# Optimization experiments

Hardware: AMD Instinct MI355X
Metric: run time of the kernel (lower is better)

The kernel has to match this reference:

```python
import jax, jax.numpy as jnp
import numpy as np

NUM_CLASSES = 80
SCORE_THR = 0.2
NMS_THR = 0.3
MAX_PER_IMAGE = 100
TOPK_PER_CLASS = 100  # cap on pre-NMS candidates per (image, class); >= max_per_image
ANCHOR_MASK = [[6, 7, 8], [3, 4, 5], [0, 1, 2]]
COCO_ANCHORS = np.array([[10, 13], [16, 30], [33, 23], [30, 61], [62, 45],
                         [59, 119], [116, 90], [156, 198], [373, 326]], dtype=np.float32)


def yolo_head(feats, layer_anchors, num_classes, input_shape):
    # feats: [B, 3*(5+C), gh, gw]
    B = feats.shape[0]
    gh, gw = feats.shape[2], feats.shape[3]
    na = layer_anchors.shape[0]
    f = feats.reshape(B, na, num_classes + 5, gh, gw).transpose(0, 3, 4, 1, 2)  # [B,gh,gw,3,5+C]
    gy, gx = jnp.meshgrid(jnp.arange(gh), jnp.arange(gw), indexing='ij')
    grid = jnp.stack([gx, gy], axis=-1).astype(f.dtype)[None, :, :, None, :]  # [1,gh,gw,1,2]
    # literal translation: divide by tensor([gh, gw]) (square grids in practice)
    box_xy = (jax.nn.sigmoid(f[..., :2]) + grid) / jnp.array([gh, gw], f.dtype)
    box_wh = jnp.exp(f[..., 2:4]) * layer_anchors[None, None, None, :, :] / input_shape[None, None, None, None, :]
    conf = jax.nn.sigmoid(f[..., 4:5])
    probs = jax.nn.sigmoid(f[..., 5:])
    return box_xy, box_wh, conf, probs


def yolo_correct_boxes(box_xy, box_wh, input_shape, image_shape):
    box_yx = box_xy[..., ::-1]
    box_hw = box_wh[..., ::-1]
    new_shape = jnp.round(image_shape * jnp.min(input_shape / image_shape))
    offset = (input_shape - new_shape) / 2.0 / input_shape
    scale = input_shape / new_shape
    box_yx = (box_yx - offset) * scale
    box_hw = box_hw * scale
    mins = box_yx - box_hw / 2.0
    maxes = box_yx + box_hw / 2.0
    boxes = jnp.concatenate([mins, maxes], axis=-1)  # (ymin, xmin, ymax, xmax)
    return boxes * jnp.concatenate([image_shape, image_shape])


def decode_layer(feats, layer_anchors, input_shape, image_shape):
    box_xy, box_wh, conf, probs = yolo_head(feats, layer_anchors, NUM_CLASSES, input_shape)
    boxes = yolo_correct_boxes(box_xy, box_wh, input_shape, image_shape)  # [B,gh,gw,3,4]
    B = feats.shape[0]
    return boxes.reshape(B, -1, 4), (conf * probs).reshape(B, -1, NUM_CLASSES)


def pairwise_iou(b):
    # b: [K,4] (y1,x1,y2,x2)
    y1, x1, y2, x2 = b[:, 0], b[:, 1], b[:, 2], b[:, 3]
    area = jnp.maximum(y2 - y1, 0) * jnp.maximum(x2 - x1, 0)
    iy1 = jnp.maximum(y1[:, None], y1[None, :])
    ix1 = jnp.maximum(x1[:, None], x1[None, :])
    iy2 = jnp.minimum(y2[:, None], y2[None, :])
    ix2 = jnp.minimum(x2[:, None], x2[None, :])
    inter = jnp.maximum(iy2 - iy1, 0) * jnp.maximum(ix2 - ix1, 0)
    return inter / (area[:, None] + area[None, :] - inter + 1e-9)


def greedy_nms(boxes, valid):
    # boxes [K,4] sorted by descending score; valid [K] bool. Returns keep mask [K].
    K = boxes.shape[0]
    iou = jax.lax.stop_gradient(pairwise_iou(boxes))
    idx = jnp.arange(K)
    def body(i, sup):
        keep_i = valid[i] & (~sup[i])
        return sup | (keep_i & (iou[i] > NMS_THR) & (idx > i))
    sup = jax.lax.fori_loop(0, K, body, jnp.zeros((K,), bool))
    return valid & (~sup)


def setup_inputs() -> dict:
    key = jax.random.key(0)
    k0, k1, k2 = jax.random.split(key, 3)
    B, F = 16, 3 * (5 + NUM_CLASSES)
    feat0 = jax.random.normal(k0, (B, F, 19, 19), jnp.float32)
    feat1 = jax.random.normal(k1, (B, F, 38, 38), jnp.float32)
    feat2 = jax.random.normal(k2, (B, F, 76, 76), jnp.float32)
    anchors = jnp.asarray(COCO_ANCHORS)
    image_shape = jnp.array([480.0, 640.0], jnp.float32)
    return {"feat0": feat0, "feat1": feat1, "feat2": feat2,
            "anchors": anchors, "image_shape": image_shape}


def reference(feat0, feat1, feat2, anchors, image_shape):
    input_shape = jnp.array([feat0.shape[2] * 32, feat0.shape[3] * 32], jnp.float32)
    feats = [feat0, feat1, feat2]
    boxes_l, scores_l = [], []
    for l in range(3):
        b, s = decode_layer(feats[l], anchors[np.array(ANCHOR_MASK[l])], input_shape, image_shape)
        boxes_l.append(b)
        scores_l.append(s)
    boxes = jnp.concatenate(boxes_l, axis=1)    # [B,N,4]
    scores = jnp.concatenate(scores_l, axis=1)  # [B,N,C]
    B = scores.shape[0]
    sc = scores.transpose(0, 2, 1)              # [B,C,N]
    top_s, top_i = jax.lax.top_k(sc, TOPK_PER_CLASS)              # [B,C,K]
    top_b = jnp.take_along_axis(boxes[:, None, :, :], top_i[..., None], axis=2)  # [B,C,K,4]
    valid = top_s >= SCORE_THR
    keep = jax.vmap(jax.vmap(greedy_nms))(top_b, valid)           # [B,C,K]
    cand = jnp.where(keep, top_s, -1.0)
    flat_s = cand.reshape(B, -1)                 # [B, C*K]
    flat_b = top_b.reshape(B, -1, 4)
    sel_s, sel_i = jax.lax.top_k(flat_s, MAX_PER_IMAGE)           # [B,100]
    sel_b = jnp.take_along_axis(flat_b, sel_i[..., None], axis=1)  # [B,100,4]
    sel_c = (sel_i // TOPK_PER_CLASS).astype(jnp.float32)
    # dets: (ymin, xmin, ymax, xmax, score, class); score == -1 marks padding
    return jnp.concatenate([sel_b, sel_s[..., None], sel_c[..., None]], axis=-1)
```

## Files before the change

### kernel.cpp

```cpp
#include <hip/hip_runtime.h>
#include <hip/hip_bf16.h>


#define NTOT   22743
#define NCLS   80
#define TOPK   100
#define KPAD   22752
#define NVEC   2842
#define Q_L1   17328
#define Q_L0   21660
#define SCORE_THR 0.2f
#define NMS_THR   0.3f

__device__ __forceinline__ float sig_exact(float x) {
    return 1.0f / (1.0f + expf(-x));
}
__device__ __forceinline__ float sig_fast(float x) {
    return __builtin_amdgcn_rcpf(1.0f + __expf(-x));
}

__global__ __launch_bounds__(256) void k_decode(
    const float* __restrict__ f0, const float* __restrict__ f1,
    const float* __restrict__ f2, const float* __restrict__ anchors,
    const float* __restrict__ imshape, float4* __restrict__ boxes,
    float* __restrict__ conf_q, int total) {
    int gid = blockIdx.x * 256 + threadIdx.x;
    if (gid >= total) return;
    int b = gid / NTOT; int p = gid - b * NTOT;

    const float* f; int ghw, gw, l, off, a, s;
    if (p < 1083)      { f=f0; off=0;    ghw=361;  gw=19; l=0; int r=p;      a=r/361;  s=r-a*361;  }
    else if (p < 5415) { f=f1; off=1083; ghw=1444; gw=38; l=1; int r=p-1083; a=r/1444; s=r-a*1444; }
    else               { f=f2; off=5415; ghw=5776; gw=76; l=2; int r=p-5415; a=r/5776; s=r-a*5776; }
    int y = s / gw, x = s - y * gw;

    const float* q = f + ((size_t)(b * 255 + a * 85) * ghw + s);
    float tx = q[0], ty = q[ghw], tw = q[2*ghw], th = q[3*ghw], tc = q[4*ghw];

    int arow = (2 - l) * 3 + a;
    float aw = anchors[arow * 2], ah = anchors[arow * 2 + 1];
    float imh = imshape[0], imw = imshape[1];
    float gf = (float)gw;

    float bxx = (sig_exact(tx) + (float)x) / gf;
    float bxy = (sig_exact(ty) + (float)y) / gf;
    float bw  = expf(tw) * aw / 608.0f;
    float bh  = expf(th) * ah / 608.0f;

    float r  = fminf(608.0f / imh, 608.0f / imw);
    float nh = rintf(imh * r), nw = rintf(imw * r);
    float offy = (608.0f - nh) / 2.0f / 608.0f;
    float offx = (608.0f - nw) / 2.0f / 608.0f;
    float scy = 608.0f / nh, scx = 608.0f / nw;

    float cy = (bxy - offy) * scy;
    float cx = (bxx - offx) * scx;
    float hh = bh * scy, ww = bw * scx;

    int n = off + 3 * s + a;
    boxes[(size_t)b * NTOT + n] =
        make_float4((cy - hh / 2.0f) * imh, (cx - ww / 2.0f) * imw,
                    (cy + hh / 2.0f) * imh, (cx + ww / 2.0f) * imw);
    int qi = (l == 2) ? (a * 5776 + s)
           : (l == 1) ? (Q_L1 + a * 1444 + s)
                      : (Q_L0 + a * 361 + s);
    conf_q[(size_t)b * KPAD + qi] = sig_exact(tc);
}

#define SEG_A  346560
#define SEG_AB 433200
#define SEG_T  519840
__global__ __launch_bounds__(256) void k_score(
    const float* __restrict__ f0, const float* __restrict__ f1,
    const float* __restrict__ f2, const float* __restrict__ conf_q,
    unsigned short* __restrict__ keybuf, int total) {
    int gid = blockIdx.x * 256 + threadIdx.x;
    if (gid >= total) return;
    const int b = gid / SEG_T;
    const int w = gid - b * SEG_T;

    if (w < SEG_AB) {
        const float* f; int a, c, s, qbase, ghw;
        if (w < SEG_A) {
            a = w / 115520; int r = w - a * 115520;
            c = r / 1444;   s = (r - c * 1444) * 4;
            f = f2; ghw = 5776; qbase = a * 5776;
        } else {
            int t = w - SEG_A;
            a = t / 28880;  int r = t - a * 28880;
            c = r / 361;    s = (r - c * 361) * 4;
            f = f1; ghw = 1444; qbase = Q_L1 + a * 1444;
        }
        const float4 lg = *(const float4*)(f + ((size_t)(b * 255 + a * 85 + 5 + c) * ghw + s));
        const float4 cf = *(const float4*)(conf_q + (size_t)b * KPAD + qbase + s);
        ushort4 k;
        k.x = (unsigned short)(__float_as_uint(cf.x * sig_fast(lg.x)) >> 16);
        k.y = (unsigned short)(__float_as_uint(cf.y * sig_fast(lg.y)) >> 16);
        k.z = (unsigned short)(__float_as_uint(cf.z * sig_fast(lg.z)) >> 16);
        k.w = (unsigned short)(__float_as_uint(cf.w * sig_fast(lg.w)) >> 16);
        *(ushort4*)(keybuf + ((size_t)(b * NCLS + c)) * KPAD + qbase + s) = k;
    } else {
        int t = w - SEG_AB;
        int a = t / 28880;  int r = t - a * 28880;
        int c = r / 361;    int s = r - c * 361;
        int qi = Q_L0 + a * 361 + s;
        float lg = f0[((size_t)(b * 255 + a * 85 + 5 + c) * 361 + s)];
        float cf = conf_q[(size_t)b * KPAD + qi];
        keybuf[((size_t)(b * NCLS + c)) * KPAD + qi] =
            (unsigned short)(__float_as_uint(cf * sig_fast(lg)) >> 16);
    }
}

__device__ void find_pivot(unsigned* hist, int H, unsigned target,
                           unsigned* suf, unsigned* sh_p, unsigned* sh_above) {
    const int tid = threadIdx.x;
    const int per = H >> 8;
    if (tid < 256) {
        unsigned acc = 0;
        for (int u = 0; u < per; ++u) acc += hist[tid * per + u];
        suf[tid] = acc;
    }
    __syncthreads();
    for (int off = 1; off < 256; off <<= 1) {
        unsigned v = 0;
        if (tid < 256) v = (tid + off < 256) ? suf[tid + off] : 0u;
        __syncthreads();
        if (tid < 256) suf[tid] += v;
        __syncthreads();
    }
    if (tid < 256) {
        unsigned mysuf = suf[tid];
        unsigned nxt = (tid == 255) ? 0u : suf[tid + 1];
        if (mysuf >= target && nxt < target) {
            unsigned above = nxt;
            for (int h = tid * per + per - 1; h >= tid * per; --h) {
                unsigned c2 = above + hist[h];
                if (c2 >= target) { *sh_p = (unsigned)h; *sh_above = above; break; }
                above = c2;
            }
        }
    }
    __syncthreads();
}

template <int TPB>
__device__ void sortT512(unsigned long long* buf) {
    const int tid = threadIdx.x;
    for (int k = 2; k <= 512; k <<= 1)
        for (int j = k >> 1; j > 0; j >>= 1) {
            __syncthreads();
            for (int i = tid; i < 512; i += TPB) {
                int ixj = i ^ j;
                if (ixj > i) {
                    unsigned long long a = buf[i], bb = buf[ixj];
                    bool desc = ((i & k) == 0);
                    if (desc ? (a < bb) : (a > bb)) { buf[i] = bb; buf[ixj] = a; }
                }
            }
        }
    __syncthreads();
}

__device__ __forceinline__ void collect_cand(
    int b, int c, int q, const float* __restrict__ f0,
    const float* __restrict__ f1, const float* __restrict__ f2,
    const float* __restrict__ conf_q, unsigned long long* buf,
    unsigned* sh_cnt) {
    int a, s, nbase, ghw;
    const float* f;
    if (q < Q_L1)      { a = q / 5776;  s = q - a * 5776;  f = f2; ghw = 5776; nbase = 5415; }
    else if (q < Q_L0) { int r = q - Q_L1; a = r / 1444; s = r - a * 1444; f = f1; ghw = 1444; nbase = 1083; }
    else               { int r = q - Q_L0; a = r / 361;  s = r - a * 361;  f = f0; ghw = 361;  nbase = 0;    }
    float t  = f[((size_t)(b * 255 + a * 85 + 5 + c)) * ghw + s];
    float cf = conf_q[(size_t)b * KPAD + q];
    float sce = cf * sig_exact(t);
    int n = nbase + 3 * s + a;
    unsigned slot = atomicAdd(sh_cnt, 1u);
    if (slot < 512)
        buf[slot] = (((unsigned long long)__float_as_uint(sce)) << 32)
                    | (unsigned)(~n);
}

__global__ __launch_bounds__(512, 8) void k_topk(
    const float* __restrict__ f0, const float* __restrict__ f1,
    const float* __restrict__ f2, const float* __restrict__ conf_q,
    const unsigned short* __restrict__ keybuf,
    const float4* __restrict__ boxes, float* __restrict__ top_s,
    float4* __restrict__ top_b) {
    __shared__ unsigned int histp[4096];
    __shared__ unsigned long long buf[512];
    __shared__ unsigned int wsum[4];
    __shared__ unsigned int sh_p, sh_above, sh_cnt;

    const int tid = threadIdx.x;
    const int row = blockIdx.x;
    const int b = row / NCLS, c = row - b * NCLS;
    const unsigned short* kr = keybuf + (size_t)row * KPAD;
    const uint4* kv = (const uint4*)kr;

    for (int i = tid; i < 4096; i += 512) histp[i] = 0;
    if (tid == 0) sh_cnt = 0;
    __syncthreads();

    for (int g = tid; g < NVEC; g += 512) {
        uint4 v = kv[g];
        unsigned ks[8] = { v.x & 0xFFFFu, v.x >> 16, v.y & 0xFFFFu, v.y >> 16,
                           v.z & 0xFFFFu, v.z >> 16, v.w & 0xFFFFu, v.w >> 16 };
        #pragma unroll
        for (int j = 0; j < 8; ++j)
            atomicAdd(&histp[ks[j] >> 2], 1u << (((ks[j] >> 1) & 1u) * 16));
    }
    if (tid < NTOT - NVEC * 8) {
        unsigned k = kr[NVEC * 8 + tid];
        atomicAdd(&histp[k >> 2], 1u << (((k >> 1) & 1u) * 16));
    }
    __syncthreads();

    {
        const int lane = tid & 63;
        unsigned own = 0;
        if (tid < 256) {
            #pragma unroll
            for (int u = 0; u < 16; ++u) {
                unsigned w = histp[tid * 16 + u];
                own += (w & 0xFFFFu) + (w >> 16);
            }
        }
        unsigned acc = own;
        #pragma unroll
        for (int d = 1; d < 64; d <<= 1) {
            unsigned v = __shfl_down(acc, d, 64);
            if (lane + d < 64) acc += v;
        }
        if (tid < 256 && lane == 0) wsum[tid >> 6] = acc;
        __syncthreads();
        if (tid < 256) {
            unsigned tail = 0;
            for (int w2 = (tid >> 6) + 1; w2 < 4; ++w2) tail += wsum[w2];
            unsigned suft = acc + tail;
            unsigned nxt  = suft - own;
            if (suft >= TOPK && nxt < TOPK) {
                unsigned above = nxt;
                for (int bb = 31; bb >= 0; --bb) {
                    unsigned w = histp[tid * 16 + (bb >> 1)];
                    unsigned cnt = (bb & 1) ? (w >> 16) : (w & 0xFFFFu);
                    if (above + cnt >= TOPK) {
                        sh_p = (unsigned)(tid * 32 + bb); sh_above = above; break;
                    }
                    above += cnt;
                }
            }
        }
        __syncthreads();
    }
    const unsigned kthr = sh_p > 0 ? ((sh_p - 1) << 1) : 0u;

    for (int g = tid; g < NVEC; g += 512) {
        uint4 v = kv[g];
        unsigned ks[8] = { v.x & 0xFFFFu, v.x >> 16, v.y & 0xFFFFu, v.y >> 16,
                           v.z & 0xFFFFu, v.z >> 16, v.w & 0xFFFFu, v.w >> 16 };
        #pragma unroll
        for (int j = 0; j < 8; ++j)
            if (ks[j] >= kthr)
                collect_cand(b, c, g * 8 + j, f0, f1, f2, conf_q, buf, &sh_cnt);
    }
    if (tid < NTOT - NVEC * 8) {
        int q = NVEC * 8 + tid;
        if ((unsigned)kr[q] >= kthr)
            collect_cand(b, c, q, f0, f1, f2, conf_q, buf, &sh_cnt);
    }
    __syncthreads();
    unsigned M = sh_cnt; if (M > 512) M = 512;
    for (int i = tid; i < 512; i += 512) if ((unsigned)i >= M) buf[i] = 0ull;
    __syncthreads();
    sortT512<512>(buf);

    if (tid < TOPK) {
        unsigned long long k = buf[tid];
        unsigned bits = (unsigned)(k >> 32);
        int n = (int)(~(unsigned)k);
        top_s[row * TOPK + tid] = __uint_as_float(bits);
        top_b[row * TOPK + tid] = boxes[(size_t)b * NTOT + n];
    }
}

__global__ __launch_bounds__(256) void k_nms(
    const float* __restrict__ top_s, const float4* __restrict__ top_b,
    float* __restrict__ cand) {
    const int lane = threadIdx.x & 63;
    const int row  = blockIdx.x * 4 + (threadIdx.x >> 6);
    const float4* bb = top_b + (size_t)row * TOPK;
    const float*  ss = top_s + (size_t)row * TOPK;

    const int j0 = lane, j1 = lane + 64;
    const bool v1 = (j1 < TOPK);
    float4 B0 = bb[j0];
    float  s0 = ss[j0];
    float4 B1 = v1 ? bb[j1] : make_float4(0.f, 0.f, 0.f, 0.f);
    float  s1 = v1 ? ss[j1] : -1.0f;
    float ar0 = fmaxf(B0.z - B0.x, 0.f) * fmaxf(B0.w - B0.y, 0.f);
    float ar1 = fmaxf(B1.z - B1.x, 0.f) * fmaxf(B1.w - B1.y, 0.f);
    int sup0 = 0, sup1 = 0;

    for (int i = 0; i < TOPK; ++i) {
        const int src = i & 63;
        const bool hi = (i >= 64);
        float yi1 = __shfl(hi ? B1.x : B0.x, src, 64);
        float xi1 = __shfl(hi ? B1.y : B0.y, src, 64);
        float yi2 = __shfl(hi ? B1.z : B0.z, src, 64);
        float xi2 = __shfl(hi ? B1.w : B0.w, src, 64);
        float si  = __shfl(hi ? s1   : s0,   src, 64);
        int  supi = __shfl(hi ? sup1 : sup0, src, 64);
        bool keep_i = (si >= SCORE_THR) && (supi == 0);
        if (keep_i) {
            float ari = fmaxf(yi2 - yi1, 0.f) * fmaxf(xi2 - xi1, 0.f);
            if (j0 > i) {
                float ty1 = fmaxf(yi1, B0.x), tx1 = fmaxf(xi1, B0.y);
                float ty2 = fminf(yi2, B0.z), tx2 = fminf(xi2, B0.w);
                float inter = fmaxf(ty2 - ty1, 0.f) * fmaxf(tx2 - tx1, 0.f);
                float iou = inter / (ari + ar0 - inter + 1e-9f);
                if (iou > NMS_THR) sup0 = 1;
            }
            if (v1 && j1 > i) {
                float ty1 = fmaxf(yi1, B1.x), tx1 = fmaxf(xi1, B1.y);
                float ty2 = fminf(yi2, B1.z), tx2 = fminf(xi2, B1.w);
                float inter = fmaxf(ty2 - ty1, 0.f) * fmaxf(tx2 - tx1, 0.f);
                float iou = inter / (ari + ar1 - inter + 1e-9f);
                if (iou > NMS_THR) sup1 = 1;
            }
        }
    }
    cand[(size_t)row * TOPK + j0] = (s0 >= SCORE_THR && sup0 == 0) ? s0 : -1.0f;
    if (v1)
        cand[(size_t)row * TOPK + j1] = (s1 >= SCORE_THR && sup1 == 0) ? s1 : -1.0f;
}

__global__ __launch_bounds__(256) void k_final(
    const float* __restrict__ cand, const float4* __restrict__ top_b,
    float* __restrict__ out) {
    __shared__ float cs[8000];
    __shared__ unsigned int hist[4096];
    __shared__ unsigned long long buf[512];
    __shared__ unsigned int suf[256];
    __shared__ unsigned int sh_kp, sh_p1, sh_above1, sh_p2, sh_above2, sh_cnt;

    const int tid = threadIdx.x, b = blockIdx.x;
    if (tid == 0) { sh_kp = 0; sh_cnt = 0; }
    for (int i = tid; i < 4096; i += 256) hist[i] = 0;
    __syncthreads();

    unsigned lk = 0;
    for (int i = tid; i < 8000; i += 256) {
        float v = cand[b * 8000 + i];
        cs[i] = v;
        if (v > -0.5f) lk++;
    }
    atomicAdd(&sh_kp, lk);
    __syncthreads();
    unsigned Kp = sh_kp;

    if (Kp >= TOPK) {
        for (int i = tid; i < 8000; i += 256)
            if (cs[i] > -0.5f) atomicAdd(&hist[__float_as_uint(cs[i]) >> 19], 1u);
        __syncthreads();
        find_pivot(hist, 2048, TOPK, suf, &sh_p1, &sh_above1);
        unsigned p1 = sh_p1, above1 = sh_above1;
        for (int i = tid; i < 4096; i += 256) hist[i] = 0;
        __syncthreads();
        for (int i = tid; i < 8000; i += 256) {
            float v = cs[i];
            if (v > -0.5f) {
                unsigned bits = __float_as_uint(v);
                if ((bits >> 19) == p1) atomicAdd(&hist[(bits >> 7) & 0xFFFu], 1u);
            }
        }
        __syncthreads();
        find_pivot(hist, 4096, TOPK - above1, suf, &sh_p2, &sh_above2);
        unsigned p2 = sh_p2;
        for (int i = tid; i < 8000; i += 256) {
            float v = cs[i];
            if (v > -0.5f) {
                unsigned bits = __float_as_uint(v);
                unsigned b1 = bits >> 19;
                if (b1 > p1 || (b1 == p1 && ((bits >> 7) & 0xFFFu) >= p2)) {
                    unsigned slot = atomicAdd(&sh_cnt, 1u);
                    if (slot < 512)
                        buf[slot] = (((unsigned long long)bits) << 32) | (unsigned)(~i);
                }
            }
        }
        __syncthreads();
        unsigned M = sh_cnt; if (M > 512) M = 512;
        for (int i = tid; i < 512; i += 256) if ((unsigned)i >= M) buf[i] = 0ull;
    } else {
        for (int i = tid; i < 512; i += 256) buf[i] = 0ull;
        __syncthreads();
        for (int i = tid; i < 8000; i += 256) {
            float v = cs[i];
            if (v > -0.5f) {
                unsigned slot = atomicAdd(&sh_cnt, 1u);
                buf[slot] = (((unsigned long long)__float_as_uint(v)) << 32) | (unsigned)(~i);
            }
        }
        __syncthreads();
        if (tid == 0) {
            unsigned need = TOPK - Kp, got = 0;
            for (int i = 0; i < 8000 && got < need; ++i)
                if (cs[i] <= -0.5f) { buf[Kp + got] = (unsigned)(~i); got++; }
        }
    }
    __syncthreads();
    sortT512<256>(buf);

    if (tid < TOPK) {
        unsigned long long k = buf[tid];
        int i = (int)(~(unsigned)k);
        int c = i / TOPK; int kk = i - c * TOPK;
        float4 bb = top_b[((size_t)b * NCLS + c) * TOPK + kk];
        int base = (b * TOPK + tid) * 6;
        out[base + 0] = bb.x; out[base + 1] = bb.y;
        out[base + 2] = bb.z; out[base + 3] = bb.w;
        out[base + 4] = cs[i]; out[base + 5] = (float)c;
    }
}

extern "C" void kernel_launch(void* const* d_in, const int* in_sizes, int n_in,
                              void* d_out, int out_size, void* d_ws, size_t ws_size,
                              hipStream_t stream) {
    (void)n_in; (void)out_size; (void)ws_size;
    const float* f0      = (const float*)d_in[0];
    const float* f1      = (const float*)d_in[1];
    const float* f2      = (const float*)d_in[2];
    const float* anchors = (const float*)d_in[3];
    const float* imshape = (const float*)d_in[4];
    const int B = in_sizes[0] / (255 * 19 * 19);

    char* ws = (char*)d_ws;
    size_t o = 0;
    unsigned short* keybuf = (unsigned short*)(ws + o);
    o += (size_t)B * NCLS * KPAD * sizeof(unsigned short);
    float4* boxes  = (float4*)(ws + o); o += (size_t)B * NTOT * sizeof(float4);
    float*  conf_q = (float*)(ws + o);  o += (size_t)B * KPAD * sizeof(float);
    float*  top_s  = (float*)(ws + o);  o += (size_t)B * NCLS * TOPK * sizeof(float);
    float4* top_b  = (float4*)(ws + o); o += (size_t)B * NCLS * TOPK * sizeof(float4);
    float*  cand   = (float*)(ws + o);  o += (size_t)B * NCLS * TOPK * sizeof(float);
    float*  out    = (float*)d_out;

    const int total = B * NTOT;
    k_decode<<<(total + 255) / 256, 256, 0, stream>>>(f0, f1, f2, anchors, imshape,
                                                      boxes, conf_q, total);
    const int stotal = B * SEG_T;
    k_score<<<(stotal + 255) / 256, 256, 0, stream>>>(f0, f1, f2, conf_q,
                                                      keybuf, stotal);
    k_topk<<<B * NCLS, 512, 0, stream>>>(f0, f1, f2, conf_q, keybuf, boxes,
                                         top_s, top_b);
    k_nms<<<(B * NCLS) / 4, 256, 0, stream>>>(top_s, top_b, cand);
    k_final<<<B, 256, 0, stream>>>(cand, top_b, out);
}
```

Measured before the change: 296.5 us.

## Fuse per-class NMS into top-k kernel and replace bitonic sort with rank counting

The separate NMS kernel is folded into the top-k kernel, so the top 100 boxes and scores are staged in shared memory and suppressed in place instead of going through a global round trip and an extra launch. The 512-element bitonic sort in both top-k and final selection is replaced by an O(M^2) rank-by-count scatter, which drops the many barrier-separated sort passes. Key vectors are loaded once into registers and reused for both histogram and collection passes rather than re-read from global. NMS now runs on one wavefront per block while the others idle, and the rank counting costs more comparisons when candidate counts are large.

```diff
diff --git a/kernel.cpp b/kernel.cpp
--- a/kernel.cpp
+++ b/kernel.cpp
@@ -140,24 +140,6 @@
             }
         }
     }
-    __syncthreads();
-}
-
-template <int TPB>
-__device__ void sortT512(unsigned long long* buf) {
-    const int tid = threadIdx.x;
-    for (int k = 2; k <= 512; k <<= 1)
-        for (int j = k >> 1; j > 0; j >>= 1) {
-            __syncthreads();
-            for (int i = tid; i < 512; i += TPB) {
-                int ixj = i ^ j;
-                if (ixj > i) {
-                    unsigned long long a = buf[i], bb = buf[ixj];
-                    bool desc = ((i & k) == 0);
-                    if (desc ? (a < bb) : (a > bb)) { buf[i] = bb; buf[ixj] = a; }
-                }
-            }
-        }
     __syncthreads();
 }
 
@@ -185,12 +167,13 @@
     const float* __restrict__ f0, const float* __restrict__ f1,
     const float* __restrict__ f2, const float* __restrict__ conf_q,
     const unsigned short* __restrict__ keybuf,
-    const float4* __restrict__ boxes, float* __restrict__ top_s,
-    float4* __restrict__ top_b) {
+    const float4* __restrict__ boxes, float4* __restrict__ top_b,
+    float* __restrict__ cand) {
     __shared__ unsigned int histp[4096];
     __shared__ unsigned long long buf[512];
     __shared__ unsigned int wsum[4];
-    __shared__ unsigned int sh_p, sh_above, sh_cnt;
+    __shared__ float sb_y1[TOPK], sb_x1[TOPK], sb_y2[TOPK], sb_x2[TOPK], sb_s[TOPK];
+    __shared__ unsigned int sh_p, sh_cnt;
 
     const int tid = threadIdx.x;
     const int row = blockIdx.x;
@@ -202,18 +185,26 @@
     if (tid == 0) sh_cnt = 0;
     __syncthreads();
 
-    for (int g = tid; g < NVEC; g += 512) {
-        uint4 v = kv[g];
-        unsigned ks[8] = { v.x & 0xFFFFu, v.x >> 16, v.y & 0xFFFFu, v.y >> 16,
-                           v.z & 0xFFFFu, v.z >> 16, v.w & 0xFFFFu, v.w >> 16 };
+    uint4 v[6];
+    bool  val[6];
+    #pragma unroll
+    for (int k = 0; k < 6; ++k) {
+        int g = tid + k * 512;
+        val[k] = (g < NVEC);
+        v[k] = val[k] ? kv[g] : make_uint4(0, 0, 0, 0);
+    }
+    const bool hastail = (tid < NTOT - NVEC * 8);
+    unsigned tailk = hastail ? (unsigned)kr[NVEC * 8 + tid] : 0u;
+
+    #pragma unroll
+    for (int k = 0; k < 6; ++k) if (val[k]) {
+        unsigned ks[8] = { v[k].x & 0xFFFFu, v[k].x >> 16, v[k].y & 0xFFFFu, v[k].y >> 16,
+                           v[k].z & 0xFFFFu, v[k].z >> 16, v[k].w & 0xFFFFu, v[k].w >> 16 };
         #pragma unroll
         for (int j = 0; j < 8; ++j)
             atomicAdd(&histp[ks[j] >> 2], 1u << (((ks[j] >> 1) & 1u) * 16));
     }
-    if (tid < NTOT - NVEC * 8) {
-        unsigned k = kr[NVEC * 8 + tid];
-        atomicAdd(&histp[k >> 2], 1u << (((k >> 1) & 1u) * 16));
-    }
+    if (hastail) atomicAdd(&histp[tailk >> 2], 1u << (((tailk >> 1) & 1u) * 16));
     __syncthreads();
 
     {
@@ -229,8 +220,8 @@
         unsigned acc = own;
         #pragma unroll
         for (int d = 1; d < 64; d <<= 1) {
-            unsigned v = __shfl_down(acc, d, 64);
-            if (lane + d < 64) acc += v;
+            unsigned vv = __shfl_down(acc, d, 64);
+            if (lane + d < 64) acc += vv;
         }
         if (tid < 256 && lane == 0) wsum[tid >> 6] = acc;
         __syncthreads();
@@ -244,9 +235,7 @@
                 for (int bb = 31; bb >= 0; --bb) {
                     unsigned w = histp[tid * 16 + (bb >> 1)];
                     unsigned cnt = (bb & 1) ? (w >> 16) : (w & 0xFFFFu);
-                    if (above + cnt >= TOPK) {
-                        sh_p = (unsigned)(tid * 32 + bb); sh_above = above; break;
-                    }
+                    if (above + cnt >= TOPK) { sh_p = (unsigned)(tid * 32 + bb); break; }
                     above += cnt;
                 }
             }
@@ -255,84 +244,73 @@
     }
     const unsigned kthr = sh_p > 0 ? ((sh_p - 1) << 1) : 0u;
 
-    for (int g = tid; g < NVEC; g += 512) {
-        uint4 v = kv[g];
-        unsigned ks[8] = { v.x & 0xFFFFu, v.x >> 16, v.y & 0xFFFFu, v.y >> 16,
-                           v.z & 0xFFFFu, v.z >> 16, v.w & 0xFFFFu, v.w >> 16 };
+    #pragma unroll
+    for (int k = 0; k < 6; ++k) if (val[k]) {
+        unsigned ks[8] = { v[k].x & 0xFFFFu, v[k].x >> 16, v[k].y & 0xFFFFu, v[k].y >> 16,
+                           v[k].z & 0xFFFFu, v[k].z >> 16, v[k].w & 0xFFFFu, v[k].w >> 16 };
         #pragma unroll
         for (int j = 0; j < 8; ++j)
             if (ks[j] >= kthr)
-                collect_cand(b, c, g * 8 + j, f0, f1, f2, conf_q, buf, &sh_cnt);
-    }
-    if (tid < NTOT - NVEC * 8) {
-        int q = NVEC * 8 + tid;
-        if ((unsigned)kr[q] >= kthr)
-            collect_cand(b, c, q, f0, f1, f2, conf_q, buf, &sh_cnt);
-    }
-    __syncthreads();
-    unsigned M = sh_cnt; if (M > 512) M = 512;
-    for (int i = tid; i < 512; i += 512) if ((unsigned)i >= M) buf[i] = 0ull;
-    __syncthreads();
-    sortT512<512>(buf);
-
-    if (tid < TOPK) {
-        unsigned long long k = buf[tid];
-        unsigned bits = (unsigned)(k >> 32);
-        int n = (int)(~(unsigned)k);
-        top_s[row * TOPK + tid] = __uint_as_float(bits);
-        top_b[row * TOPK + tid] = boxes[(size_t)b * NTOT + n];
-    }
-}
-
-__global__ __launch_bounds__(256) void k_nms(
-    const float* __restrict__ top_s, const float4* __restrict__ top_b,
-    float* __restrict__ cand) {
-    const int lane = threadIdx.x & 63;
-    const int row  = blockIdx.x * 4 + (threadIdx.x >> 6);
-    const float4* bb = top_b + (size_t)row * TOPK;
-    const float*  ss = top_s + (size_t)row * TOPK;
-
-    const int j0 = lane, j1 = lane + 64;
-    const bool v1 = (j1 < TOPK);
-    float4 B0 = bb[j0];
-    float  s0 = ss[j0];
-    float4 B1 = v1 ? bb[j1] : make_float4(0.f, 0.f, 0.f, 0.f);
-    float  s1 = v1 ? ss[j1] : -1.0f;
-    float ar0 = fmaxf(B0.z - B0.x, 0.f) * fmaxf(B0.w - B0.y, 0.f);
-    float ar1 = fmaxf(B1.z - B1.x, 0.f) * fmaxf(B1.w - B1.y, 0.f);
-    int sup0 = 0, sup1 = 0;
-
-    for (int i = 0; i < TOPK; ++i) {
-        const int src = i & 63;
-        const bool hi = (i >= 64);
-        float yi1 = __shfl(hi ? B1.x : B0.x, src, 64);
-        float xi1 = __shfl(hi ? B1.y : B0.y, src, 64);
-        float yi2 = __shfl(hi ? B1.z : B0.z, src, 64);
-        float xi2 = __shfl(hi ? B1.w : B0.w, src, 64);
-        float si  = __shfl(hi ? s1   : s0,   src, 64);
-        int  supi = __shfl(hi ? sup1 : sup0, src, 64);
-        bool keep_i = (si >= SCORE_THR) && (supi == 0);
-        if (keep_i) {
-            float ari = fmaxf(yi2 - yi1, 0.f) * fmaxf(xi2 - xi1, 0.f);
-            if (j0 > i) {
-                float ty1 = fmaxf(yi1, B0.x), tx1 = fmaxf(xi1, B0.y);
-                float ty2 = fminf(yi2, B0.z), tx2 = fminf(xi2, B0.w);
-                float inter = fmaxf(ty2 - ty1, 0.f) * fmaxf(tx2 - tx1, 0.f);
-                float iou = inter / (ari + ar0 - inter + 1e-9f);
-                if (iou > NMS_THR) sup0 = 1;
-            }
-            if (v1 && j1 > i) {
-                float ty1 = fmaxf(yi1, B1.x), tx1 = fmaxf(xi1, B1.y);
-                float ty2 = fminf(yi2, B1.z), tx2 = fminf(xi2, B1.w);
-                float inter = fmaxf(ty2 - ty1, 0.f) * fmaxf(tx2 - tx1, 0.f);
-                float iou = inter / (ari + ar1 - inter + 1e-9f);
-                if (iou > NMS_THR) sup1 = 1;
-            }
-        }
-    }
-    cand[(size_t)row * TOPK + j0] = (s0 >= SCORE_THR && sup0 == 0) ? s0 : -1.0f;
-    if (v1)
-        cand[(size_t)row * TOPK + j1] = (s1 >= SCORE_THR && sup1 == 0) ? s1 : -1.0f;
+                collect_cand(b, c, (tid + k * 512) * 8 + j, f0, f1, f2, conf_q, buf, &sh_cnt);
+    }
+    if (hastail && tailk >= kthr)
+        collect_cand(b, c, NVEC * 8 + tid, f0, f1, f2, conf_q, buf, &sh_cnt);
+    __syncthreads();
+
+    const int M = (int)min(sh_cnt, 512u);
+    if (tid < M) {
+        unsigned long long mykey = buf[tid];
+        int rank = 0;
+        for (int j = 0; j < M; ++j) rank += (buf[j] > mykey);
+        if (rank < TOPK) {
+            int n = (int)(~(unsigned)mykey);
+            float4 bx = boxes[(size_t)b * NTOT + n];
+            sb_y1[rank] = bx.x; sb_x1[rank] = bx.y;
+            sb_y2[rank] = bx.z; sb_x2[rank] = bx.w;
+            sb_s[rank]  = __uint_as_float((unsigned)(mykey >> 32));
+            top_b[(size_t)row * TOPK + rank] = bx;
+        }
+    }
+    __syncthreads();
+
+    if (tid < 64) {
+        const int j0 = tid, j1 = tid + 64;
+        const bool v1 = (j1 < TOPK);
+        float y10 = sb_y1[j0], x10 = sb_x1[j0], y20 = sb_y2[j0], x20 = sb_x2[j0];
+        float s0 = sb_s[j0];
+        float y11 = v1 ? sb_y1[j1] : 0.f, x11 = v1 ? sb_x1[j1] : 0.f;
+        float y21 = v1 ? sb_y2[j1] : 0.f, x21 = v1 ? sb_x2[j1] : 0.f;
+        float s1 = v1 ? sb_s[j1] : -1.0f;
+        float ar0 = fmaxf(y20 - y10, 0.f) * fmaxf(x20 - x10, 0.f);
+        float ar1 = fmaxf(y21 - y11, 0.f) * fmaxf(x21 - x11, 0.f);
+        int sup0 = 0, sup1 = 0;
+        for (int i = 0; i < TOPK; ++i) {
+            float yi1 = sb_y1[i], xi1 = sb_x1[i], yi2 = sb_y2[i], xi2 = sb_x2[i];
+            float si = sb_s[i];
+            int supi = (i < 64) ? __shfl(sup0, i, 64) : __shfl(sup1, i - 64, 64);
+            bool keep_i = (si >= SCORE_THR) && (supi == 0);
+            if (keep_i) {
+                float ari = fmaxf(yi2 - yi1, 0.f) * fmaxf(xi2 - xi1, 0.f);
+                if (j0 > i) {
+                    float ty1 = fmaxf(yi1, y10), tx1 = fmaxf(xi1, x10);
+                    float ty2 = fminf(yi2, y20), tx2 = fminf(xi2, x20);
+                    float inter = fmaxf(ty2 - ty1, 0.f) * fmaxf(tx2 - tx1, 0.f);
+                    float iou = inter / (ari + ar0 - inter + 1e-9f);
+                    if (iou > NMS_THR) sup0 = 1;
+                }
+                if (v1 && j1 > i) {
+                    float ty1 = fmaxf(yi1, y11), tx1 = fmaxf(xi1, x11);
+                    float ty2 = fminf(yi2, y21), tx2 = fminf(xi2, x21);
+                    float inter = fmaxf(ty2 - ty1, 0.f) * fmaxf(tx2 - tx1, 0.f);
+                    float iou = inter / (ari + ar1 - inter + 1e-9f);
+                    if (iou > NMS_THR) sup1 = 1;
+                }
+            }
+        }
+        cand[(size_t)row * TOPK + j0] = (s0 >= SCORE_THR && sup0 == 0) ? s0 : -1.0f;
+        if (v1)
+            cand[(size_t)row * TOPK + j1] = (s1 >= SCORE_THR && sup1 == 0) ? s1 : -1.0f;
+    }
 }
 
 __global__ __launch_bounds__(256) void k_final(
@@ -389,12 +367,7 @@
                 }
             }
         }
-        __syncthreads();
-        unsigned M = sh_cnt; if (M > 512) M = 512;
-        for (int i = tid; i < 512; i += 256) if ((unsigned)i >= M) buf[i] = 0ull;
     } else {
-        for (int i = tid; i < 512; i += 256) buf[i] = 0ull;
-        __syncthreads();
         for (int i = tid; i < 8000; i += 256) {
             float v = cs[i];
             if (v > -0.5f) {
@@ -410,17 +383,21 @@
         }
     }
     __syncthreads();
-    sortT512<256>(buf);
-
-    if (tid < TOPK) {
-        unsigned long long k = buf[tid];
-        int i = (int)(~(unsigned)k);
-        int c = i / TOPK; int kk = i - c * TOPK;
-        float4 bb = top_b[((size_t)b * NCLS + c) * TOPK + kk];
-        int base = (b * TOPK + tid) * 6;
-        out[base + 0] = bb.x; out[base + 1] = bb.y;
-        out[base + 2] = bb.z; out[base + 3] = bb.w;
-        out[base + 4] = cs[i]; out[base + 5] = (float)c;
+
+    const int M2 = (Kp >= TOPK) ? (int)min(sh_cnt, 512u) : (int)TOPK;
+    for (int i = tid; i < M2; i += 256) {
+        unsigned long long key = buf[i];
+        int rank = 0;
+        for (int j = 0; j < M2; ++j) rank += (buf[j] > key);
+        if (rank < TOPK) {
+            int fi = (int)(~(unsigned)key);
+            int c = fi / TOPK; int kk = fi - c * TOPK;
+            float4 bb = top_b[((size_t)b * NCLS + c) * TOPK + kk];
+            int base = (b * TOPK + rank) * 6;
+            out[base + 0] = bb.x; out[base + 1] = bb.y;
+            out[base + 2] = bb.z; out[base + 3] = bb.w;
+            out[base + 4] = cs[fi]; out[base + 5] = (float)c;
+        }
     }
 }
 
@@ -441,7 +418,6 @@
     o += (size_t)B * NCLS * KPAD * sizeof(unsigned short);
     float4* boxes  = (float4*)(ws + o); o += (size_t)B * NTOT * sizeof(float4);
     float*  conf_q = (float*)(ws + o);  o += (size_t)B * KPAD * sizeof(float);
-    float*  top_s  = (float*)(ws + o);  o += (size_t)B * NCLS * TOPK * sizeof(float);
     float4* top_b  = (float4*)(ws + o); o += (size_t)B * NCLS * TOPK * sizeof(float4);
     float*  cand   = (float*)(ws + o);  o += (size_t)B * NCLS * TOPK * sizeof(float);
     float*  out    = (float*)d_out;
@@ -453,7 +429,6 @@
     k_score<<<(stotal + 255) / 256, 256, 0, stream>>>(f0, f1, f2, conf_q,
                                                       keybuf, stotal);
     k_topk<<<B * NCLS, 512, 0, stream>>>(f0, f1, f2, conf_q, keybuf, boxes,
-                                         top_s, top_b);
-    k_nms<<<(B * NCLS) / 4, 256, 0, stream>>>(top_s, top_b, cand);
+                                         top_b, cand);
     k_final<<<B, 256, 0, stream>>>(cand, top_b, out);
 }
```

Measured after the change: 265.7 us. 1.12x faster.
